# Kernel optimization log

Measured on AMD Instinct MI355X. Metric: run time of the kernel, lower is better.

## Reference

```python
import jax, jax.numpy as jnp
import numpy as np

B, T, C, NH = 4, 2048, 1024, 16
HS = C // NH


def setup_inputs() -> dict:
    key = jax.random.key(0)
    k1, k2, k3, k4, k5 = jax.random.split(key, 5)
    s = 1.0 / np.sqrt(C)
    return {
        "x": jax.random.normal(k1, (B, T, C), dtype=jnp.float32),
        "Wqkv": jax.random.normal(k2, (3 * C, C), dtype=jnp.float32) * s,
        "bqkv": jax.random.normal(k3, (3 * C,), dtype=jnp.float32) * 0.02,
        "Wproj": jax.random.normal(k4, (C, C), dtype=jnp.float32) * s,
        "bproj": jax.random.normal(k5, (C,), dtype=jnp.float32) * 0.02,
    }


def reference(x, Wqkv, bqkv, Wproj, bproj):
    Bsz, Tlen, Cdim = x.shape
    # qkv projection (torch Linear: x @ W.T + b)
    qkv = x @ Wqkv.T + bqkv                      # [B, T, 3C]
    q, k, v = jnp.split(qkv, 3, axis=-1)
    # [B, NH, T, HS]
    q = q.reshape(Bsz, Tlen, NH, HS).transpose(0, 2, 1, 3)
    k = k.reshape(Bsz, Tlen, NH, HS).transpose(0, 2, 1, 3)
    v = v.reshape(Bsz, Tlen, NH, HS).transpose(0, 2, 1, 3)
    scale = 1.0 / np.sqrt(HS)
    att = jnp.einsum('bhqd,bhkd->bhqk', q, k) * scale
    causal = jnp.triu(jnp.ones((Tlen, Tlen), dtype=bool), k=1)
    att = jnp.where(causal[None, None], -jnp.inf, att)
    att = jax.nn.softmax(att, axis=-1)
    y = jnp.einsum('bhqk,bhkd->bhqd', att, v)    # [B, NH, T, HS]
    y = y.transpose(0, 2, 1, 3).reshape(Bsz, Tlen, Cdim)
    return y @ Wproj.T + bproj
```

## Files before the change

### kernel.cpp

```cpp
#include <hip/hip_runtime.h>
#include <hip/hip_bf16.h>

#define B_   4
#define T_   2048
#define C_   1024
#define NH_  16
#define HS_  64
#define M_   8192
#define N1_  3072
#define BH_  64

typedef __attribute__((ext_vector_type(8))) short short8;
typedef __attribute__((ext_vector_type(4))) short short4v;
typedef __attribute__((ext_vector_type(4))) float f32x4;

#define QSCALE 0.18033688011112042f

__device__ __forceinline__ short f2bf(float f) {
  unsigned u = __float_as_uint(f);
  unsigned r = (u + 0x7fffu + ((u >> 16) & 1u)) >> 16;
  return (short)r;
}
__device__ __forceinline__ unsigned pk_bf16(float a, float b) {
  __hip_bfloat162 h = __float22bfloat162_rn(make_float2(a, b));
  union { __hip_bfloat162 h2; unsigned u; } cv; cv.h2 = h; return cv.u;
}

typedef __attribute__((address_space(1))) unsigned int as1_uint;
typedef __attribute__((address_space(3))) unsigned int as3_uint;
__device__ __forceinline__ void g2l16(const void* g, void* l) {
  __builtin_amdgcn_global_load_lds((as1_uint*)g, (as3_uint*)l, 16, 0, 0);
}

__global__ __launch_bounds__(256) void conv_bf16(
    const float* __restrict__ src, short* __restrict__ dst)
{
  const size_t i = ((size_t)blockIdx.x * 256 + threadIdx.x) * 8;
  const f32x4 a = *(const f32x4*)&src[i];
  const f32x4 b = *(const f32x4*)&src[i + 4];
  short8 o;
  o[0] = f2bf(a[0]); o[1] = f2bf(a[1]); o[2] = f2bf(a[2]); o[3] = f2bf(a[3]);
  o[4] = f2bf(b[0]); o[5] = f2bf(b[1]); o[6] = f2bf(b[2]); o[7] = f2bf(b[3]);
  *(short8*)&dst[i] = o;
}

__global__ __launch_bounds__(256) void qkv_gemm(
    const short* __restrict__ X,
    const short* __restrict__ W,
    const float* __restrict__ bias,
    short* __restrict__ Qo, short* __restrict__ Ko, short* __restrict__ Vt)
{
  __shared__ short As[2][128 * 64];
  __shared__ short Bs[2][128 * 64];
  const int tid = threadIdx.x;
  const int lane = tid & 63;
  const int wid = tid >> 6;
  const int wy = wid >> 1, wx = wid & 1;
  const int lq = lane >> 4, lm = lane & 15;
  const int row0 = blockIdx.x * 128;
  const int col0 = blockIdx.y * 128;

  f32x4 acc[4][4] = {};

  const int ar = tid >> 3;
  const int ac = (tid & 7) << 3;

#pragma unroll
  for (int j = 0; j < 4; ++j) {
    const int r = ar + j * 32;
    g2l16(&X[(size_t)(row0 + r) * C_ + ac], &As[0][r * 64 + ac]);
    g2l16(&W[(size_t)(col0 + r) * C_ + ac], &Bs[0][r * 64 + ac]);
  }
  __syncthreads();

  int cur = 0;
  for (int k0 = 0; k0 < C_; k0 += 64) {
    if (k0 + 64 < C_) {
#pragma unroll
      for (int j = 0; j < 4; ++j) {
        const int r = ar + j * 32;
        g2l16(&X[(size_t)(row0 + r) * C_ + k0 + 64 + ac], &As[cur ^ 1][r * 64 + ac]);
        g2l16(&W[(size_t)(col0 + r) * C_ + k0 + 64 + ac], &Bs[cur ^ 1][r * 64 + ac]);
      }
    }

#pragma unroll
    for (int kk = 0; kk < 2; ++kk) {
      short8 af[4], bfr[4];
#pragma unroll
      for (int mi = 0; mi < 4; ++mi)
        af[mi] = *(const short8*)&As[cur][(wy * 64 + mi * 16 + lm) * 64 + kk * 32 + lq * 8];
#pragma unroll
      for (int ni = 0; ni < 4; ++ni)
        bfr[ni] = *(const short8*)&Bs[cur][(wx * 64 + ni * 16 + lm) * 64 + kk * 32 + lq * 8];
#pragma unroll
      for (int mi = 0; mi < 4; ++mi)
#pragma unroll
        for (int ni = 0; ni < 4; ++ni)
          acc[mi][ni] = __builtin_amdgcn_mfma_f32_16x16x32_bf16(af[mi], bfr[ni], acc[mi][ni], 0, 0, 0);
    }

    __syncthreads();
    cur ^= 1;
  }

#pragma unroll
  for (int ni = 0; ni < 4; ++ni) {
    const int n = col0 + wx * 64 + ni * 16 + lm;
    const float bv = bias[n];
    const int sel = n >> 10;
    const int cc = n & (C_ - 1);
    const int h = cc >> 6, d = cc & 63;
    if (sel == 2) {
#pragma unroll
      for (int mi = 0; mi < 4; ++mi) {
        const int m0 = row0 + wy * 64 + mi * 16 + lq * 4;
        const int b = m0 >> 11, t0 = m0 & (T_ - 1);
        const int bh = b * NH_ + h;
        short4v o;
#pragma unroll
        for (int i = 0; i < 4; ++i) o[i] = f2bf(acc[mi][ni][i] + bv);
        *(short4v*)&Vt[((size_t)bh * HS_ + d) * T_ + t0] = o;
      }
    } else {
      short* dst = (sel == 0) ? Qo : Ko;
      const float qs = (sel == 0) ? QSCALE : 1.0f;
#pragma unroll
      for (int mi = 0; mi < 4; ++mi) {
#pragma unroll
        for (int i = 0; i < 4; ++i) {
          const int m = row0 + wy * 64 + mi * 16 + lq * 4 + i;
          const int b = m >> 11, t = m & (T_ - 1);
          const int bh = b * NH_ + h;
          dst[((size_t)bh * T_ + t) * HS_ + d] = f2bf((acc[mi][ni][i] + bv) * qs);
        }
      }
    }
  }
}

__global__ __launch_bounds__(256) void proj_gemm(
    const short* __restrict__ Y,
    const short* __restrict__ W,
    const float* __restrict__ bias,
    float* __restrict__ Out)
{
  __shared__ short As[2][128 * 64];
  __shared__ short Bs[2][128 * 64];
  const int tid = threadIdx.x;
  const int lane = tid & 63;
  const int wid = tid >> 6;
  const int wy = wid >> 1, wx = wid & 1;
  const int lq = lane >> 4, lm = lane & 15;
  const int row0 = blockIdx.x * 128;
  const int col0 = blockIdx.y * 128;

  f32x4 acc[4][4] = {};

  const int ar = tid >> 3;
  const int ac = (tid & 7) << 3;

#pragma unroll
  for (int j = 0; j < 4; ++j) {
    const int r = ar + j * 32;
    g2l16(&Y[(size_t)(row0 + r) * C_ + ac], &As[0][r * 64 + ac]);
    g2l16(&W[(size_t)(col0 + r) * C_ + ac], &Bs[0][r * 64 + ac]);
  }
  __syncthreads();

  int cur = 0;
  for (int k0 = 0; k0 < C_; k0 += 64) {
    if (k0 + 64 < C_) {
#pragma unroll
      for (int j = 0; j < 4; ++j) {
        const int r = ar + j * 32;
        g2l16(&Y[(size_t)(row0 + r) * C_ + k0 + 64 + ac], &As[cur ^ 1][r * 64 + ac]);
        g2l16(&W[(size_t)(col0 + r) * C_ + k0 + 64 + ac], &Bs[cur ^ 1][r * 64 + ac]);
      }
    }

#pragma unroll
    for (int kk = 0; kk < 2; ++kk) {
      short8 af[4], bfr[4];
#pragma unroll
      for (int mi = 0; mi < 4; ++mi)
        af[mi] = *(const short8*)&As[cur][(wy * 64 + mi * 16 + lm) * 64 + kk * 32 + lq * 8];
#pragma unroll
      for (int ni = 0; ni < 4; ++ni)
        bfr[ni] = *(const short8*)&Bs[cur][(wx * 64 + ni * 16 + lm) * 64 + kk * 32 + lq * 8];
#pragma unroll
      for (int mi = 0; mi < 4; ++mi)
#pragma unroll
        for (int ni = 0; ni < 4; ++ni)
          acc[mi][ni] = __builtin_amdgcn_mfma_f32_16x16x32_bf16(af[mi], bfr[ni], acc[mi][ni], 0, 0, 0);
    }

    __syncthreads();
    cur ^= 1;
  }

#pragma unroll
  for (int ni = 0; ni < 4; ++ni) {
    const int n = col0 + wx * 64 + ni * 16 + lm;
    const float bv = bias[n];
#pragma unroll
    for (int mi = 0; mi < 4; ++mi) {
#pragma unroll
      for (int i = 0; i < 4; ++i) {
        const int m = row0 + wy * 64 + mi * 16 + lq * 4 + i;
        Out[(size_t)m * C_ + n] = acc[mi][ni][i] + bv;
      }
    }
  }
}

#define LDK 72
__global__ __launch_bounds__(256) void attn(
    const short* __restrict__ Qg, const short* __restrict__ Kg,
    const short* __restrict__ Vg, short* __restrict__ Yo)
{
  __shared__ short Ks[64 * LDK];
  __shared__ short Vs[64 * LDK];

  const int tid = threadIdx.x;
  const int lane = tid & 63;
  const int w = tid >> 6;
  const int lq = lane >> 4, lm = lane & 15;
  const int bh = blockIdx.y;
  const int b = bh >> 4, h = bh & 15;
  const size_t base = (size_t)bh * T_ * HS_;
  const short* __restrict__ Kb = Kg + base;
  const short* __restrict__ Vb = Vg + base;

  const int sr = tid >> 3;
  const int sc = (tid & 7) * 8;

#pragma unroll 1
  for (int half = 0; half < 2; ++half) {
    const int qt = half ? (int)blockIdx.x : 15 - (int)blockIdx.x;
    const int q0 = qt * 128;
    const int qA = q0 + w * 16 + lm;
    const int qB = qA + 64;

    const short8 qfA0 = *(const short8*)&Qg[base + (size_t)qA * HS_ + lq * 8];
    const short8 qfA1 = *(const short8*)&Qg[base + (size_t)qA * HS_ + 32 + lq * 8];
    const short8 qfB0 = *(const short8*)&Qg[base + (size_t)qB * HS_ + lq * 8];
    const short8 qfB1 = *(const short8*)&Qg[base + (size_t)qB * HS_ + 32 + lq * 8];

    float lA = 0.0f, lB = 0.0f;
    f32x4 oA[4] = {}, oB[4] = {};

    const int nkt = 2 * qt + 2;

    short8 pk0 = *(const short8*)&Kb[(size_t)sr * HS_ + sc];
    short8 pk1 = *(const short8*)&Kb[(size_t)(32 + sr) * HS_ + sc];
    short8 pv0 = *(const short8*)&Vb[(size_t)sr * T_ + sc];
    short8 pv1 = *(const short8*)&Vb[(size_t)(32 + sr) * T_ + sc];

#pragma unroll 1
    for (int kt = 0; kt < nkt; ++kt) {
      const int kv0 = kt * 64;

      __syncthreads();
      *(short8*)&Ks[sr * LDK + sc] = pk0;
      *(short8*)&Ks[(32 + sr) * LDK + sc] = pk1;
      *(short8*)&Vs[sr * LDK + sc] = pv0;
      *(short8*)&Vs[(32 + sr) * LDK + sc] = pv1;
      __syncthreads();

      if (kt + 1 < nkt) {
        const int nk = kv0 + 64;
        pk0 = *(const short8*)&Kb[(size_t)(nk + sr) * HS_ + sc];
        pk1 = *(const short8*)&Kb[(size_t)(nk + 32 + sr) * HS_ + sc];
        pv0 = *(const short8*)&Vb[(size_t)sr * T_ + nk + sc];
        pv1 = *(const short8*)&Vb[(size_t)(32 + sr) * T_ + nk + sc];
      }

      const bool doA = (kt <= 2 * qt);

      short8 kf0[4], kf1[4];
#pragma unroll
      for (int ni = 0; ni < 4; ++ni) {
        kf0[ni] = *(const short8*)&Ks[(ni * 16 + lm) * LDK + lq * 8];
        kf1[ni] = *(const short8*)&Ks[(ni * 16 + lm) * LDK + 32 + lq * 8];
      }

      f32x4 svA[4], svB[4];
      if (doA) {
#pragma unroll
        for (int ni = 0; ni < 4; ++ni) {
          f32x4 s = {};
          s = __builtin_amdgcn_mfma_f32_16x16x32_bf16(kf0[ni], qfA0, s, 0, 0, 0);
          svA[ni] = __builtin_amdgcn_mfma_f32_16x16x32_bf16(kf1[ni], qfA1, s, 0, 0, 0);
        }
      }
#pragma unroll
      for (int ni = 0; ni < 4; ++ni) {
        f32x4 s = {};
        s = __builtin_amdgcn_mfma_f32_16x16x32_bf16(kf0[ni], qfB0, s, 0, 0, 0);
        svB[ni] = __builtin_amdgcn_mfma_f32_16x16x32_bf16(kf1[ni], qfB1, s, 0, 0, 0);
      }

      if (kt == 2 * qt) {
#pragma unroll
        for (int ni = 0; ni < 4; ++ni) {
          const int kvb = kv0 + ni * 16 + lq * 4;
#pragma unroll
          for (int i = 0; i < 4; ++i)
            if (kvb + i > qA) svA[ni][i] = -3.0e38f;
        }
      }
      if (kt == 2 * qt + 1) {
#pragma unroll
        for (int ni = 0; ni < 4; ++ni) {
          const int kvb = kv0 + ni * 16 + lq * 4;
#pragma unroll
          for (int i = 0; i < 4; ++i)
            if (kvb + i > qB) svB[ni][i] = -3.0e38f;
        }
      }

      short4v p4A[4], p4B[4];
      if (doA) {
#pragma unroll
        for (int ni = 0; ni < 4; ++ni)
#pragma unroll
          for (int i = 0; i < 4; ++i)
            svA[ni][i] = __builtin_amdgcn_exp2f(svA[ni][i]);
        lA += ((svA[0][0] + svA[0][1]) + (svA[0][2] + svA[0][3]))
            + ((svA[1][0] + svA[1][1]) + (svA[1][2] + svA[1][3]))
            + ((svA[2][0] + svA[2][1]) + (svA[2][2] + svA[2][3]))
            + ((svA[3][0] + svA[3][1]) + (svA[3][2] + svA[3][3]));
#pragma unroll
        for (int ni = 0; ni < 4; ++ni) {
          union { short4v s4; unsigned u[2]; } pk;
          pk.u[0] = pk_bf16(svA[ni][0], svA[ni][1]);
          pk.u[1] = pk_bf16(svA[ni][2], svA[ni][3]);
          p4A[ni] = pk.s4;
        }
      }
#pragma unroll
      for (int ni = 0; ni < 4; ++ni)
#pragma unroll
        for (int i = 0; i < 4; ++i)
          svB[ni][i] = __builtin_amdgcn_exp2f(svB[ni][i]);
      lB += ((svB[0][0] + svB[0][1]) + (svB[0][2] + svB[0][3]))
          + ((svB[1][0] + svB[1][1]) + (svB[1][2] + svB[1][3]))
          + ((svB[2][0] + svB[2][1]) + (svB[2][2] + svB[2][3]))
          + ((svB[3][0] + svB[3][1]) + (svB[3][2] + svB[3][3]));
#pragma unroll
      for (int ni = 0; ni < 4; ++ni) {
        union { short4v s4; unsigned u[2]; } pk;
        pk.u[0] = pk_bf16(svB[ni][0], svB[ni][1]);
        pk.u[1] = pk_bf16(svB[ni][2], svB[ni][3]);
        p4B[ni] = pk.s4;
      }

      if (doA) {
#pragma unroll
        for (int di = 0; di < 4; ++di) {
#pragma unroll
          for (int ni = 0; ni < 4; ++ni) {
            const short4v vfr = *(const short4v*)&Vs[(di * 16 + lm) * LDK + ni * 16 + lq * 4];
            oA[di] = __builtin_amdgcn_mfma_f32_16x16x16bf16_1k(vfr, p4A[ni], oA[di], 0, 0, 0);
            oB[di] = __builtin_amdgcn_mfma_f32_16x16x16bf16_1k(vfr, p4B[ni], oB[di], 0, 0, 0);
          }
        }
      } else {
#pragma unroll
        for (int di = 0; di < 4; ++di) {
#pragma unroll
          for (int ni = 0; ni < 4; ++ni) {
            const short4v vfr = *(const short4v*)&Vs[(di * 16 + lm) * LDK + ni * 16 + lq * 4];
            oB[di] = __builtin_amdgcn_mfma_f32_16x16x16bf16_1k(vfr, p4B[ni], oB[di], 0, 0, 0);
          }
        }
      }
    }

    lA += __shfl_xor(lA, 16);
    lA += __shfl_xor(lA, 32);
    lB += __shfl_xor(lB, 16);
    lB += __shfl_xor(lB, 32);
    const float rlA = 1.0f / lA;
    const float rlB = 1.0f / lB;
    const size_t rowA = ((size_t)(b * T_ + qA)) * C_ + h * HS_;
    const size_t rowB = ((size_t)(b * T_ + qB)) * C_ + h * HS_;
#pragma unroll
    for (int di = 0; di < 4; ++di) {
      union { short4v s4; unsigned u[2]; } pk;
      pk.u[0] = pk_bf16(oA[di][0] * rlA, oA[di][1] * rlA);
      pk.u[1] = pk_bf16(oA[di][2] * rlA, oA[di][3] * rlA);
      *(short4v*)&Yo[rowA + di * 16 + lq * 4] = pk.s4;
      pk.u[0] = pk_bf16(oB[di][0] * rlB, oB[di][1] * rlB);
      pk.u[1] = pk_bf16(oB[di][2] * rlB, oB[di][3] * rlB);
      *(short4v*)&Yo[rowB + di * 16 + lq * 4] = pk.s4;
    }
  }
}

extern "C" void kernel_launch(void* const* d_in, const int* in_sizes, int n_in,
                              void* d_out, int out_size, void* d_ws, size_t ws_size,
                              hipStream_t stream) {
  (void)in_sizes; (void)n_in; (void)out_size;
  const float* x     = (const float*)d_in[0];
  const float* Wqkv  = (const float*)d_in[1];
  const float* bqkv  = (const float*)d_in[2];
  const float* Wproj = (const float*)d_in[3];
  const float* bproj = (const float*)d_in[4];
  float* out = (float*)d_out;

  const size_t nWq = (size_t)N1_ * C_;
  const size_t nWp = (size_t)C_ * C_;
  const size_t nFull = (size_t)M_ * C_;
  const size_t nB = (size_t)T_ * C_;

  dim3 blk(256);
  const size_t need_batched = (nWq + nWp + 4 * nFull) * sizeof(short);

  if (ws_size >= need_batched) {
    short* Wq_bf = (short*)d_ws;
    short* Wp_bf = Wq_bf + nWq;
    short* S0    = Wp_bf + nWp;
    short* Qw    = S0 + nFull;
    short* Kw    = Qw + nFull;
    short* Vw    = Kw + nFull;

    conv_bf16<<<dim3((int)(nWq / 2048)), blk, 0, stream>>>(Wqkv, Wq_bf);
    conv_bf16<<<dim3((int)(nWp / 2048)), blk, 0, stream>>>(Wproj, Wp_bf);
    conv_bf16<<<dim3((int)(nFull / 2048)), blk, 0, stream>>>(x, S0);
    qkv_gemm<<<dim3(M_ / 128, N1_ / 128), blk, 0, stream>>>(S0, Wq_bf, bqkv, Qw, Kw, Vw);
    attn<<<dim3(8, BH_), blk, 0, stream>>>(Qw, Kw, Vw, S0);
    proj_gemm<<<dim3(M_ / 128, C_ / 128), blk, 0, stream>>>(S0, Wp_bf, bproj, out);
  } else {
    short* Wq_bf = (short*)d_ws;
    short* Wp_bf = Wq_bf + nWq;
    short* S0    = Wp_bf + nWp;
    short* Qw    = S0 + nB;
    short* Kw    = Qw + nB;
    short* Vw    = Kw + nB;

    conv_bf16<<<dim3((int)(nWq / 2048)), blk, 0, stream>>>(Wqkv, Wq_bf);
    conv_bf16<<<dim3((int)(nWp / 2048)), blk, 0, stream>>>(Wproj, Wp_bf);
    for (int b = 0; b < B_; ++b) {
      const float* xb = x   + (size_t)b * nB;
      float*       ob = out + (size_t)b * nB;
      conv_bf16<<<dim3((int)(nB / 2048)), blk, 0, stream>>>(xb, S0);
      qkv_gemm<<<dim3(T_ / 128, N1_ / 128), blk, 0, stream>>>(S0, Wq_bf, bqkv, Qw, Kw, Vw);
      attn<<<dim3(8, NH_), blk, 0, stream>>>(Qw, Kw, Vw, S0);
      proj_gemm<<<dim3(T_ / 128, C_ / 128), blk, 0, stream>>>(S0, Wp_bf, bproj, ob);
    }
  }
}
```

Baseline: 262.5 us.

## Run both causal query tiles concurrently in one 512-thread attention block

The attention kernel used to process two query tiles (a long and a short causal tile) one after the other in a 256-thread block. Now a 512-thread block runs both tiles at once as two 4-wave groups that share each K/V tile loaded into LDS, so every thread loads only one short8 of K and one of V. The grid is transposed so blockIdx.x indexes batch-head, placing blocks of the same head next to each other. The cost is that the short-tile group sits idle through the barriers while the long tile finishes, and the launch bound is set to 512 threads with a minimum of 4 blocks.

```diff
diff --git a/kernel.cpp b/kernel.cpp
--- a/kernel.cpp
+++ b/kernel.cpp
@@ -215,7 +215,7 @@
 }
 
 #define LDK 72
-__global__ __launch_bounds__(256) void attn(
+__global__ __launch_bounds__(512, 4) void attn(
     const short* __restrict__ Qg, const short* __restrict__ Kg,
     const short* __restrict__ Vg, short* __restrict__ Yo)
 {
@@ -225,8 +225,10 @@
   const int tid = threadIdx.x;
   const int lane = tid & 63;
   const int w = tid >> 6;
+  const int wq = w & 3;
+  const int grp = w >> 2;
   const int lq = lane >> 4, lm = lane & 15;
-  const int bh = blockIdx.y;
+  const int bh = blockIdx.x;
   const int b = bh >> 4, h = bh & 15;
   const size_t base = (size_t)bh * T_ * HS_;
   const short* __restrict__ Kb = Kg + base;
@@ -235,47 +237,40 @@
   const int sr = tid >> 3;
   const int sc = (tid & 7) * 8;
 
+  const int ty = blockIdx.y;
+  const int qt = grp ? ty : (15 - ty);
+  const int nkt_g = 2 * qt + 2;
+  const int nktA = 32 - 2 * ty;
+
+  const int qA = qt * 128 + wq * 16 + lm;
+  const int qB = qA + 64;
+
+  const short8 qfA0 = *(const short8*)&Qg[base + (size_t)qA * HS_ + lq * 8];
+  const short8 qfA1 = *(const short8*)&Qg[base + (size_t)qA * HS_ + 32 + lq * 8];
+  const short8 qfB0 = *(const short8*)&Qg[base + (size_t)qB * HS_ + lq * 8];
+  const short8 qfB1 = *(const short8*)&Qg[base + (size_t)qB * HS_ + 32 + lq * 8];
+
+  float lA = 0.0f, lB = 0.0f;
+  f32x4 oA[4] = {}, oB[4] = {};
+
+  short8 pk = *(const short8*)&Kb[(size_t)sr * HS_ + sc];
+  short8 pv = *(const short8*)&Vb[(size_t)sr * T_ + sc];
+
 #pragma unroll 1
-  for (int half = 0; half < 2; ++half) {
-    const int qt = half ? (int)blockIdx.x : 15 - (int)blockIdx.x;
-    const int q0 = qt * 128;
-    const int qA = q0 + w * 16 + lm;
-    const int qB = qA + 64;
-
-    const short8 qfA0 = *(const short8*)&Qg[base + (size_t)qA * HS_ + lq * 8];
-    const short8 qfA1 = *(const short8*)&Qg[base + (size_t)qA * HS_ + 32 + lq * 8];
-    const short8 qfB0 = *(const short8*)&Qg[base + (size_t)qB * HS_ + lq * 8];
-    const short8 qfB1 = *(const short8*)&Qg[base + (size_t)qB * HS_ + 32 + lq * 8];
-
-    float lA = 0.0f, lB = 0.0f;
-    f32x4 oA[4] = {}, oB[4] = {};
-
-    const int nkt = 2 * qt + 2;
-
-    short8 pk0 = *(const short8*)&Kb[(size_t)sr * HS_ + sc];
-    short8 pk1 = *(const short8*)&Kb[(size_t)(32 + sr) * HS_ + sc];
-    short8 pv0 = *(const short8*)&Vb[(size_t)sr * T_ + sc];
-    short8 pv1 = *(const short8*)&Vb[(size_t)(32 + sr) * T_ + sc];
-
-#pragma unroll 1
-    for (int kt = 0; kt < nkt; ++kt) {
-      const int kv0 = kt * 64;
-
-      __syncthreads();
-      *(short8*)&Ks[sr * LDK + sc] = pk0;
-      *(short8*)&Ks[(32 + sr) * LDK + sc] = pk1;
-      *(short8*)&Vs[sr * LDK + sc] = pv0;
-      *(short8*)&Vs[(32 + sr) * LDK + sc] = pv1;
-      __syncthreads();
-
-      if (kt + 1 < nkt) {
-        const int nk = kv0 + 64;
-        pk0 = *(const short8*)&Kb[(size_t)(nk + sr) * HS_ + sc];
-        pk1 = *(const short8*)&Kb[(size_t)(nk + 32 + sr) * HS_ + sc];
-        pv0 = *(const short8*)&Vb[(size_t)sr * T_ + nk + sc];
-        pv1 = *(const short8*)&Vb[(size_t)(32 + sr) * T_ + nk + sc];
-      }
-
+  for (int kt = 0; kt < nktA; ++kt) {
+    const int kv0 = kt * 64;
+
+    __syncthreads();
+    *(short8*)&Ks[sr * LDK + sc] = pk;
+    *(short8*)&Vs[sr * LDK + sc] = pv;
+    __syncthreads();
+
+    if (kt + 1 < nktA) {
+      pk = *(const short8*)&Kb[(size_t)(kv0 + 64 + sr) * HS_ + sc];
+      pv = *(const short8*)&Vb[(size_t)sr * T_ + kv0 + 64 + sc];
+    }
+
+    if (kt < nkt_g) {
       const bool doA = (kt <= 2 * qt);
 
       short8 kf0[4], kf1[4];
@@ -333,10 +328,10 @@
             + ((svA[3][0] + svA[3][1]) + (svA[3][2] + svA[3][3]));
 #pragma unroll
         for (int ni = 0; ni < 4; ++ni) {
-          union { short4v s4; unsigned u[2]; } pk;
-          pk.u[0] = pk_bf16(svA[ni][0], svA[ni][1]);
-          pk.u[1] = pk_bf16(svA[ni][2], svA[ni][3]);
-          p4A[ni] = pk.s4;
+          union { short4v s4; unsigned u[2]; } pk2;
+          pk2.u[0] = pk_bf16(svA[ni][0], svA[ni][1]);
+          pk2.u[1] = pk_bf16(svA[ni][2], svA[ni][3]);
+          p4A[ni] = pk2.s4;
         }
       }
 #pragma unroll
@@ -350,10 +345,10 @@
           + ((svB[3][0] + svB[3][1]) + (svB[3][2] + svB[3][3]));
 #pragma unroll
       for (int ni = 0; ni < 4; ++ni) {
-        union { short4v s4; unsigned u[2]; } pk;
-        pk.u[0] = pk_bf16(svB[ni][0], svB[ni][1]);
-        pk.u[1] = pk_bf16(svB[ni][2], svB[ni][3]);
-        p4B[ni] = pk.s4;
+        union { short4v s4; unsigned u[2]; } pk2;
+        pk2.u[0] = pk_bf16(svB[ni][0], svB[ni][1]);
+        pk2.u[1] = pk_bf16(svB[ni][2], svB[ni][3]);
+        p4B[ni] = pk2.s4;
       }
 
       if (doA) {
@@ -377,25 +372,25 @@
         }
       }
     }
-
-    lA += __shfl_xor(lA, 16);
-    lA += __shfl_xor(lA, 32);
-    lB += __shfl_xor(lB, 16);
-    lB += __shfl_xor(lB, 32);
-    const float rlA = 1.0f / lA;
-    const float rlB = 1.0f / lB;
-    const size_t rowA = ((size_t)(b * T_ + qA)) * C_ + h * HS_;
-    const size_t rowB = ((size_t)(b * T_ + qB)) * C_ + h * HS_;
-#pragma unroll
-    for (int di = 0; di < 4; ++di) {
-      union { short4v s4; unsigned u[2]; } pk;
-      pk.u[0] = pk_bf16(oA[di][0] * rlA, oA[di][1] * rlA);
-      pk.u[1] = pk_bf16(oA[di][2] * rlA, oA[di][3] * rlA);
-      *(short4v*)&Yo[rowA + di * 16 + lq * 4] = pk.s4;
-      pk.u[0] = pk_bf16(oB[di][0] * rlB, oB[di][1] * rlB);
-      pk.u[1] = pk_bf16(oB[di][2] * rlB, oB[di][3] * rlB);
-      *(short4v*)&Yo[rowB + di * 16 + lq * 4] = pk.s4;
-    }
+  }
+
+  lA += __shfl_xor(lA, 16);
+  lA += __shfl_xor(lA, 32);
+  lB += __shfl_xor(lB, 16);
+  lB += __shfl_xor(lB, 32);
+  const float rlA = 1.0f / lA;
+  const float rlB = 1.0f / lB;
+  const size_t rowA = ((size_t)(b * T_ + qA)) * C_ + h * HS_;
+  const size_t rowB = ((size_t)(b * T_ + qB)) * C_ + h * HS_;
+#pragma unroll
+  for (int di = 0; di < 4; ++di) {
+    union { short4v s4; unsigned u[2]; } pk2;
+    pk2.u[0] = pk_bf16(oA[di][0] * rlA, oA[di][1] * rlA);
+    pk2.u[1] = pk_bf16(oA[di][2] * rlA, oA[di][3] * rlA);
+    *(short4v*)&Yo[rowA + di * 16 + lq * 4] = pk2.s4;
+    pk2.u[0] = pk_bf16(oB[di][0] * rlB, oB[di][1] * rlB);
+    pk2.u[1] = pk_bf16(oB[di][2] * rlB, oB[di][3] * rlB);
+    *(short4v*)&Yo[rowB + di * 16 + lq * 4] = pk2.s4;
   }
 }
 
@@ -430,7 +425,7 @@
     conv_bf16<<<dim3((int)(nWp / 2048)), blk, 0, stream>>>(Wproj, Wp_bf);
     conv_bf16<<<dim3((int)(nFull / 2048)), blk, 0, stream>>>(x, S0);
     qkv_gemm<<<dim3(M_ / 128, N1_ / 128), blk, 0, stream>>>(S0, Wq_bf, bqkv, Qw, Kw, Vw);
-    attn<<<dim3(8, BH_), blk, 0, stream>>>(Qw, Kw, Vw, S0);
+    attn<<<dim3(BH_, 8), dim3(512), 0, stream>>>(Qw, Kw, Vw, S0);
     proj_gemm<<<dim3(M_ / 128, C_ / 128), blk, 0, stream>>>(S0, Wp_bf, bproj, out);
   } else {
     short* Wq_bf = (short*)d_ws;
@@ -447,7 +442,7 @@
       float*       ob = out + (size_t)b * nB;
       conv_bf16<<<dim3((int)(nB / 2048)), blk, 0, stream>>>(xb, S0);
       qkv_gemm<<<dim3(T_ / 128, N1_ / 128), blk, 0, stream>>>(S0, Wq_bf, bqkv, Qw, Kw, Vw);
-      attn<<<dim3(8, NH_), blk, 0, stream>>>(Qw, Kw, Vw, S0);
+      attn<<<dim3(NH_, 8), dim3(512), 0, stream>>>(Qw, Kw, Vw, S0);
       proj_gemm<<<dim3(T_ / 128, C_ / 128), blk, 0, stream>>>(S0, Wp_bf, bproj, ob);
     }
   }
```

New measurement: 258.2 us. Within noise of the previous version (-1.6%).
